# Performance work log

Measured on AMD Instinct MI355X. Metric: run time of the kernel, lower is better.

## Reference

```python
import jax, jax.numpy as jnp
import numpy as np

NEG = -1e30  # stand-in for -inf that keeps gradients finite


def setup_inputs() -> dict:
    key = jax.random.key(0)
    k0, k1, k2 = jax.random.split(key, 3)
    B, S, W, K = 48, 128, 4, 256
    logits = jax.random.normal(k0, (B, S, W, K), dtype=jnp.float32)
    T = jax.random.normal(k1, (B, K, K), dtype=jnp.float32)
    hamming_cost = jax.random.uniform(k2, (B, S, W, K), dtype=jnp.float32)
    tag_mask = jnp.ones((B, K, K), dtype=jnp.float32)
    text_mask = jnp.ones((B, S), dtype=jnp.int32)
    return dict(logits=logits, T=T, hamming_cost=hamming_cost,
                tag_mask=tag_mask, text_mask=text_mask)


def reference(logits, T, hamming_cost, tag_mask, text_mask):
    # Semi-Markov CRF partition function (use_transition_layer == 'True').
    B, S, W, K = logits.shape
    lg = jnp.transpose(logits, (1, 2, 0, 3))        # (S, W, B, K)
    hc = jnp.transpose(hamming_cost, (1, 2, 0, 3))  # (S, W, B, K)
    # emission score for a span of width w+1 ending at j, labeled k
    emit_all = (lg + hc) * tag_mask[:, 0, :]        # (S, W, B, K)
    tranT = T * tag_mask                            # (B, K, Kprev)
    w_idx = jnp.arange(W)

    # buf[w] = alpha[j - w]; rows with j - w < 0 held at NEG (excluded)
    buf0 = jnp.full((W, B, K), NEG, dtype=jnp.float32).at[0].set(0.0)

    def step(buf, inp):
        emit_j, j = inp  # emit_j: (W, B, K)
        # transition applies only when the previous alpha is a real segment
        # boundary (w < j); the w == j row connects to the initial state.
        tran = jnp.where((w_idx < j)[:, None, None, None], tranT[None], 0.0)
        # scores[w, b, k, kp] = alpha[j-w, b, kp] + T'[b, k, kp] + emit[w, b, k]
        scores = buf[:, :, None, :] + tran + emit_j[:, :, :, None]
        alpha_j = jax.nn.logsumexp(scores, axis=(0, 3))  # (B, K)
        buf = jnp.concatenate([alpha_j[None], buf[:-1]], axis=0)
        return buf, alpha_j

    _, alphas = jax.lax.scan(step, buf0, (emit_all, jnp.arange(S)))
    full = jnp.concatenate([jnp.zeros((1, B, K), dtype=jnp.float32), alphas], axis=0)
    ls = jax.nn.logsumexp(full, axis=-1)            # (S+1, B)
    lengths = jnp.sum(text_mask, axis=1)            # (B,)
    partition = ls[lengths, jnp.arange(B)]          # (B,)
    return partition[None]                          # (1, B) as in torch code
```

## Files before the change

kernel.cpp:

```cpp
#include <hip/hip_runtime.h>
#include <hip/hip_bf16.h>
#include <type_traits>

typedef __attribute__((ext_vector_type(8))) _Float16 half8;
typedef __attribute__((ext_vector_type(4))) _Float16 half4;
typedef __attribute__((ext_vector_type(4))) float f32x4;

constexpr int CB = 48, CS = 128, CW = 4, CK = 256;
constexpr int LDP = 264;

__global__ void prep_eT_kernel(const f32x4* __restrict__ T,
                               const f32x4* __restrict__ tm,
                               half4* __restrict__ eT, int n4) {
    int i = blockIdx.x * 256 + threadIdx.x;
    if (i < n4) {
        f32x4 t = T[i], m = tm[i];
        half4 o;
        o[0] = (_Float16)__expf(t[0] * m[0]);
        o[1] = (_Float16)__expf(t[1] * m[1]);
        o[2] = (_Float16)__expf(t[2] * m[2]);
        o[3] = (_Float16)__expf(t[3] * m[3]);
        eT[i] = o;
    }
}

__global__ __launch_bounds__(256, 1)
void crf_scan_kernel(const float* __restrict__ logits,
                     const float* __restrict__ ham,
                     const _Float16* __restrict__ eT,
                     const float* __restrict__ tag_mask,
                     const int* __restrict__ text_mask,
                     float* __restrict__ out) {
    const int b = blockIdx.x;
    const int tid = (int)threadIdx.x;
    const int wv = tid >> 6;
    const int lane = tid & 63;
    const int l16 = lane & 15;
    const int g4 = lane >> 4;

    __shared__ alignas(16) _Float16 ebuf[4 * LDP];
    __shared__ float red[4];
    __shared__ int len_s;

    if (tid == 0) len_s = 0;
    __syncthreads();
    if (tid < CS) atomicAdd(&len_s, text_mask[b * CS + tid]);
    ebuf[3 * LDP + tid] = (_Float16)1.0f;

    const float tm0 = tag_mask[(size_t)b * CK * CK + tid];

    half8 bfr[8][4];
    const _Float16* eTb = eT + (size_t)b * CK * CK;
#pragma unroll
    for (int c = 0; c < 8; ++c)
#pragma unroll
        for (int t = 0; t < 4; ++t) {
            int k = wv * 64 + t * 16 + l16;
            bfr[c][t] = *(const half8*)(eTb + (size_t)k * CK + c * 32 + g4 * 8);
        }

    const float* lgb = logits + (size_t)b * CS * CW * CK;
    const float* hcb = ham    + (size_t)b * CS * CW * CK;

    half8 af[8];
    {
        const _Float16 iv = ((l16 & 3) == 3) ? (_Float16)1.0f : (_Float16)0.0f;
        half8 v;
#pragma unroll
        for (int i = 0; i < 8; ++i) v[i] = iv;
#pragma unroll
        for (int c = 0; c < 8; ++c) af[c] = v;
    }

    float mr[4] = {0.0f, 0.0f, 0.0f, 0.0f};
    float ls_prev = __logf(256.0f) - 2.0f;
    float out_r = __logf(256.0f);
    float e_last = 0.0f, M_last = 0.0f;
    float Mcur = __logf(256.0f) + 2.0f;
    float scl  = __expf(0.0f - Mcur);

    float lgp[4][4], hcp[4][4];
#pragma unroll
    for (int s = 0; s < 4; ++s)
#pragma unroll
        for (int w = 0; w < 4; ++w) {
            int idx = s * (CW * CK) + w * CK + tid;
            lgp[s][w] = lgb[idx];
            hcp[s][w] = hcb[idx];
        }

    __syncthreads();
    const int len = len_s;

    half8 ones;
#pragma unroll
    for (int i = 0; i < 8; ++i) ones[i] = (_Float16)1.0f;

    auto step = [&](int j, auto uc, auto firstc) {
        constexpr int u = uc.value;
        constexpr bool first = firstc.value;
        constexpr int sp = (u + 3) & 3;

        if ((l16 & 3) == sp) {
#pragma unroll
            for (int c = 0; c < 8; ++c)
                af[c] = *(const half8*)(ebuf + sp * LDP + c * 32 + g4 * 8);
        }

        float em_w[4];
#pragma unroll
        for (int w = 0; w < 4; ++w)
            em_w[w] = (lgp[u][w] + hcp[u][w]) * tm0;

        {
            int jn = (j + 4 < CS) ? j + 4 : 0;
#pragma unroll
            for (int w = 0; w < 4; ++w) {
                int idx = jn * (CW * CK) + w * CK + tid;
                lgp[u][w] = lgb[idx];
                hcp[u][w] = hcb[idx];
            }
        }

        const float C = mr[sp];
        float E[4];
#pragma unroll
        for (int r = 0; r < 4; ++r)
            E[r] = __expf(mr[r] + em_w[(u + 3 - r) & 3] - C);
        mr[u] = Mcur;

        f32x4 acc[4];
#pragma unroll
        for (int t = 0; t < 4; ++t) acc[t] = (f32x4){0.0f, 0.0f, 0.0f, 0.0f};
        f32x4 s0 = {0, 0, 0, 0}, s1 = {0, 0, 0, 0};
#pragma unroll
        for (int c = 0; c < 8; ++c) {
#pragma unroll
            for (int t = 0; t < 4; ++t)
                acc[t] = __builtin_amdgcn_mfma_f32_16x16x32_f16(af[c], bfr[c][t], acc[t], 0, 0, 0);
            if (c & 1) s1 = __builtin_amdgcn_mfma_f32_16x16x32_f16(af[c], ones, s1, 0, 0, 0);
            else       s0 = __builtin_amdgcn_mfma_f32_16x16x32_f16(af[c], ones, s0, 0, 0, 0);
        }
        f32x4 rsum = s0 + s1;

        float S = 0.0f;
#pragma unroll
        for (int r = 0; r < 4; ++r) {
            float v01 = (g4 & 1) ? acc[1][r] : acc[0][r];
            float v23 = (g4 & 1) ? acc[3][r] : acc[2][r];
            float yv  = (g4 & 2) ? v23 : v01;
            if (first) {
                const int w = (u + 3 - r) & 3;
                if (w == j) yv = 256.0f;
                else if (w > j) yv = 0.0f;
            }
            S = fmaf(yv, E[r], S);
        }
        float e = S * scl;
        ebuf[u * LDP + tid] = (_Float16)e;
        e_last = e;
        M_last = Mcur;

        float lsj = C + __logf(rsum[sp]);
        if (j == len) out_r = lsj;
        float delta = lsj - ls_prev;
        ls_prev = lsj;
        float Mn = lsj + 2.0f * delta;
        scl = __expf(Mcur - Mn);
        Mcur = Mn;

        asm volatile("s_waitcnt lgkmcnt(0)" ::: "memory");
        __builtin_amdgcn_s_barrier();
        __builtin_amdgcn_sched_barrier(0);
    };

#define IC(v) std::integral_constant<int, v>{}
#define BC(v) std::integral_constant<bool, v>{}
    step(0, IC(0), BC(true));
    step(1, IC(1), BC(true));
    step(2, IC(2), BC(true));
    step(3, IC(3), BC(true));
    for (int jj = 4; jj < CS; jj += 4) {
        step(jj + 0, IC(0), BC(false));
        step(jj + 1, IC(1), BC(false));
        step(jj + 2, IC(2), BC(false));
        step(jj + 3, IC(3), BC(false));
    }
#undef IC
#undef BC

    float s = e_last;
#pragma unroll
    for (int o = 32; o; o >>= 1) s += __shfl_xor(s, o, 64);
    if (lane == 0) red[wv] = s;
    __syncthreads();
    if (tid == 0) {
        float tot = red[0] + red[1] + red[2] + red[3];
        float ls_full = M_last + __logf(tot);
        if (len == CS) out_r = ls_full;
        out[b] = out_r;
    }
}

extern "C" void kernel_launch(void* const* d_in, const int* in_sizes, int n_in,
                              void* d_out, int out_size, void* d_ws, size_t ws_size,
                              hipStream_t stream) {
    const float* logits    = (const float*)d_in[0];
    const float* T         = (const float*)d_in[1];
    const float* ham       = (const float*)d_in[2];
    const float* tag_mask  = (const float*)d_in[3];
    const int*   text_mask = (const int*)d_in[4];
    float* out = (float*)d_out;

    _Float16* eT = (_Float16*)d_ws;
    int n4 = CB * CK * CK / 4;
    prep_eT_kernel<<<(n4 + 255) / 256, 256, 0, stream>>>(
        (const f32x4*)T, (const f32x4*)tag_mask, (half4*)eT, n4);
    crf_scan_kernel<<<CB, 256, 0, stream>>>(logits, ham, eT, tag_mask, text_mask, out);
}
```

Before: 176.7 us.

## Defer log-sum update to next step and split MFMA accumulation chains

Moves the per-step logsumexp/rescale computation (log, exp, Mcur update) out of the critical path after the MFMA chain and into the start of the following step, so it overlaps the LDS load of the A fragments. It also splits the MFMA accumulation into two independent accumulator sets over the K halves, which shortens dependent MFMA chains. The cost is extra accumulator registers and an added vector add, plus careful handling of the last step's output.

Result: slower. 182.8 us (+3.5%).

```diff
diff --git a/kernel.cpp b/kernel.cpp
--- a/kernel.cpp
+++ b/kernel.cpp
@@ -78,6 +78,7 @@
     float e_last = 0.0f, M_last = 0.0f;
     float Mcur = __logf(256.0f) + 2.0f;
     float scl  = __expf(0.0f - Mcur);
+    float rs_prev = 0.0f, C_trail = 0.0f;
 
     float lgp[4][4], hcp[4][4];
 #pragma unroll
@@ -100,11 +101,22 @@
         constexpr int u = uc.value;
         constexpr bool first = firstc.value;
         constexpr int sp = (u + 3) & 3;
+        constexpr bool do_trail = !(first && u == 0);
 
         if ((l16 & 3) == sp) {
 #pragma unroll
             for (int c = 0; c < 8; ++c)
                 af[c] = *(const half8*)(ebuf + sp * LDP + c * 32 + g4 * 8);
+        }
+
+        if constexpr (do_trail) {
+            float lsj = C_trail + __logf(rs_prev);
+            if (j - 1 == len) out_r = lsj;
+            float delta = lsj - ls_prev;
+            ls_prev = lsj;
+            float Mn = lsj + 2.0f * delta;
+            scl = __expf(Mcur - Mn);
+            Mcur = Mn;
         }
 
         float em_w[4];
@@ -129,19 +141,31 @@
             E[r] = __expf(mr[r] + em_w[(u + 3 - r) & 3] - C);
         mr[u] = Mcur;
 
+        f32x4 accA[4], accB[4];
+#pragma unroll
+        for (int t = 0; t < 4; ++t) {
+            accA[t] = (f32x4){0.0f, 0.0f, 0.0f, 0.0f};
+            accB[t] = (f32x4){0.0f, 0.0f, 0.0f, 0.0f};
+        }
+        f32x4 s0 = {0, 0, 0, 0}, s1 = {0, 0, 0, 0};
+#pragma unroll
+        for (int c = 0; c < 4; ++c) {
+#pragma unroll
+            for (int t = 0; t < 4; ++t)
+                accA[t] = __builtin_amdgcn_mfma_f32_16x16x32_f16(af[c], bfr[c][t], accA[t], 0, 0, 0);
+            s0 = __builtin_amdgcn_mfma_f32_16x16x32_f16(af[c], ones, s0, 0, 0, 0);
+        }
+#pragma unroll
+        for (int c = 4; c < 8; ++c) {
+#pragma unroll
+            for (int t = 0; t < 4; ++t)
+                accB[t] = __builtin_amdgcn_mfma_f32_16x16x32_f16(af[c], bfr[c][t], accB[t], 0, 0, 0);
+            s1 = __builtin_amdgcn_mfma_f32_16x16x32_f16(af[c], ones, s1, 0, 0, 0);
+        }
+        f32x4 rsum = s0 + s1;
         f32x4 acc[4];
 #pragma unroll
-        for (int t = 0; t < 4; ++t) acc[t] = (f32x4){0.0f, 0.0f, 0.0f, 0.0f};
-        f32x4 s0 = {0, 0, 0, 0}, s1 = {0, 0, 0, 0};
-#pragma unroll
-        for (int c = 0; c < 8; ++c) {
-#pragma unroll
-            for (int t = 0; t < 4; ++t)
-                acc[t] = __builtin_amdgcn_mfma_f32_16x16x32_f16(af[c], bfr[c][t], acc[t], 0, 0, 0);
-            if (c & 1) s1 = __builtin_amdgcn_mfma_f32_16x16x32_f16(af[c], ones, s1, 0, 0, 0);
-            else       s0 = __builtin_amdgcn_mfma_f32_16x16x32_f16(af[c], ones, s0, 0, 0, 0);
-        }
-        f32x4 rsum = s0 + s1;
+        for (int t = 0; t < 4; ++t) acc[t] = accA[t] + accB[t];
 
         float S = 0.0f;
 #pragma unroll
@@ -161,13 +185,8 @@
         e_last = e;
         M_last = Mcur;
 
-        float lsj = C + __logf(rsum[sp]);
-        if (j == len) out_r = lsj;
-        float delta = lsj - ls_prev;
-        ls_prev = lsj;
-        float Mn = lsj + 2.0f * delta;
-        scl = __expf(Mcur - Mn);
-        Mcur = Mn;
+        C_trail = C;
+        rs_prev = rsum[sp];
 
         asm volatile("s_waitcnt lgkmcnt(0)" ::: "memory");
         __builtin_amdgcn_s_barrier();
@@ -189,6 +208,11 @@
 #undef IC
 #undef BC
 
+    {
+        float lsj = C_trail + __logf(rs_prev);
+        if (len == CS - 1) out_r = lsj;
+    }
+
     float s = e_last;
 #pragma unroll
     for (int o = 32; o; o >>= 1) s += __shfl_xor(s, o, 64);
```

## Replace per-step MFMA matvec with per-thread fdot2 row dot products

Applied to the files above, without the earlier changes.

Each thread now keeps its full row of exp(T) in registers (32 half8) and computes its row dot product against the previous alpha row with packed fp16 fdot2 instructions, caching the result per window slot. This replaces the MFMA-based matvec, where most of each 16-row A tile was wasted because only one row held real data. The row sum still uses a small MFMA against a ones vector. The new path needs many more VGPRs (256 halves of T plus 256 halves of alpha broadcast-read from LDS each step), and serial fdot2 chains of 256 elements per thread may make the dependent-step latency longer.

After: 208.2 us. 17.8% more time.

```diff
diff --git a/kernel.cpp b/kernel.cpp
--- a/kernel.cpp
+++ b/kernel.cpp
@@ -4,6 +4,7 @@
 
 typedef __attribute__((ext_vector_type(8))) _Float16 half8;
 typedef __attribute__((ext_vector_type(4))) _Float16 half4;
+typedef __attribute__((ext_vector_type(2))) _Float16 half2;
 typedef __attribute__((ext_vector_type(4))) float f32x4;
 
 constexpr int CB = 48, CS = 128, CW = 4, CK = 256;
@@ -35,7 +36,6 @@
     const int tid = (int)threadIdx.x;
     const int wv = tid >> 6;
     const int lane = tid & 63;
-    const int l16 = lane & 15;
     const int g4 = lane >> 4;
 
     __shared__ alignas(16) _Float16 ebuf[4 * LDP];
@@ -49,28 +49,17 @@
 
     const float tm0 = tag_mask[(size_t)b * CK * CK + tid];
 
-    half8 bfr[8][4];
-    const _Float16* eTb = eT + (size_t)b * CK * CK;
-#pragma unroll
-    for (int c = 0; c < 8; ++c)
-#pragma unroll
-        for (int t = 0; t < 4; ++t) {
-            int k = wv * 64 + t * 16 + l16;
-            bfr[c][t] = *(const half8*)(eTb + (size_t)k * CK + c * 32 + g4 * 8);
-        }
+    half8 et[32];
+    {
+        const _Float16* eTr = eT + (size_t)b * CK * CK + (size_t)tid * CK;
+#pragma unroll
+        for (int i = 0; i < 32; ++i) et[i] = *(const half8*)(eTr + 8 * i);
+    }
 
     const float* lgb = logits + (size_t)b * CS * CW * CK;
     const float* hcb = ham    + (size_t)b * CS * CW * CK;
 
-    half8 af[8];
-    {
-        const _Float16 iv = ((l16 & 3) == 3) ? (_Float16)1.0f : (_Float16)0.0f;
-        half8 v;
-#pragma unroll
-        for (int i = 0; i < 8; ++i) v[i] = iv;
-#pragma unroll
-        for (int c = 0; c < 8; ++c) af[c] = v;
-    }
+    float Y[4] = {0.0f, 0.0f, 0.0f, 0.0f};
 
     float mr[4] = {0.0f, 0.0f, 0.0f, 0.0f};
     float ls_prev = __logf(256.0f) - 2.0f;
@@ -101,11 +90,19 @@
         constexpr bool first = firstc.value;
         constexpr int sp = (u + 3) & 3;
 
-        if ((l16 & 3) == sp) {
-#pragma unroll
-            for (int c = 0; c < 8; ++c)
-                af[c] = *(const half8*)(ebuf + sp * LDP + c * 32 + g4 * 8);
-        }
+        const _Float16* rowp = ebuf + sp * LDP;
+
+        half8 er[32];
+#pragma unroll
+        for (int i = 0; i < 32; ++i) er[i] = *(const half8*)(rowp + 8 * i);
+        half8 saf[8];
+#pragma unroll
+        for (int c = 0; c < 8; ++c) saf[c] = *(const half8*)(rowp + c * 32 + g4 * 8);
+
+        f32x4 sacc = (f32x4){0.0f, 0.0f, 0.0f, 0.0f};
+#pragma unroll
+        for (int c = 0; c < 8; ++c)
+            sacc = __builtin_amdgcn_mfma_f32_16x16x32_f16(saf[c], ones, sacc, 0, 0, 0);
 
         float em_w[4];
 #pragma unroll
@@ -129,26 +126,30 @@
             E[r] = __expf(mr[r] + em_w[(u + 3 - r) & 3] - C);
         mr[u] = Mcur;
 
-        f32x4 acc[4];
-#pragma unroll
-        for (int t = 0; t < 4; ++t) acc[t] = (f32x4){0.0f, 0.0f, 0.0f, 0.0f};
-        f32x4 s0 = {0, 0, 0, 0}, s1 = {0, 0, 0, 0};
-#pragma unroll
-        for (int c = 0; c < 8; ++c) {
-#pragma unroll
-            for (int t = 0; t < 4; ++t)
-                acc[t] = __builtin_amdgcn_mfma_f32_16x16x32_f16(af[c], bfr[c][t], acc[t], 0, 0, 0);
-            if (c & 1) s1 = __builtin_amdgcn_mfma_f32_16x16x32_f16(af[c], ones, s1, 0, 0, 0);
-            else       s0 = __builtin_amdgcn_mfma_f32_16x16x32_f16(af[c], ones, s0, 0, 0, 0);
-        }
-        f32x4 rsum = s0 + s1;
+        float a0 = 0, a1 = 0, a2 = 0, a3 = 0, a4 = 0, a5 = 0, a6 = 0, a7 = 0;
+#pragma unroll
+        for (int i = 0; i < 32; ++i) {
+#pragma unroll
+            for (int q = 0; q < 4; ++q) {
+                half2 ep = {er[i][2 * q], er[i][2 * q + 1]};
+                half2 tp = {et[i][2 * q], et[i][2 * q + 1]};
+                const int c = (i * 4 + q) & 7;
+                if (c == 0) a0 = __builtin_amdgcn_fdot2(ep, tp, a0, false);
+                else if (c == 1) a1 = __builtin_amdgcn_fdot2(ep, tp, a1, false);
+                else if (c == 2) a2 = __builtin_amdgcn_fdot2(ep, tp, a2, false);
+                else if (c == 3) a3 = __builtin_amdgcn_fdot2(ep, tp, a3, false);
+                else if (c == 4) a4 = __builtin_amdgcn_fdot2(ep, tp, a4, false);
+                else if (c == 5) a5 = __builtin_amdgcn_fdot2(ep, tp, a5, false);
+                else if (c == 6) a6 = __builtin_amdgcn_fdot2(ep, tp, a6, false);
+                else a7 = __builtin_amdgcn_fdot2(ep, tp, a7, false);
+            }
+        }
+        Y[sp] = ((a0 + a4) + (a1 + a5)) + ((a2 + a6) + (a3 + a7));
 
         float S = 0.0f;
 #pragma unroll
         for (int r = 0; r < 4; ++r) {
-            float v01 = (g4 & 1) ? acc[1][r] : acc[0][r];
-            float v23 = (g4 & 1) ? acc[3][r] : acc[2][r];
-            float yv  = (g4 & 2) ? v23 : v01;
+            float yv = Y[r];
             if (first) {
                 const int w = (u + 3 - r) & 3;
                 if (w == j) yv = 256.0f;
@@ -161,7 +162,8 @@
         e_last = e;
         M_last = Mcur;
 
-        float lsj = C + __logf(rsum[sp]);
+        float sum_prev = sacc[0];
+        float lsj = C + __logf(sum_prev);
         if (j == len) out_r = lsj;
         float delta = lsj - ls_prev;
         ls_prev = lsj;
```
